# Performance work log

Measured on AMD Instinct MI355X. Metric: run time of the kernel, lower is better.

Reference implementation:

```python
import jax, jax.numpy as jnp
import numpy as np

C_CURV = 1.0
EPS = 1e-5            # bound_eps from source
MAX_NORM = (1.0 - 1e-5) / (C_CURV ** 0.5)  # Poincare ball projection radius


def _conv3x3(x, w, b):
    # x: (N,Cin,H,W), w: (Cout,Cin,3,3), padding=1 -> SAME
    y = jax.lax.conv_general_dilated(
        x, w, window_strides=(1, 1), padding=((1, 1), (1, 1)),
        dimension_numbers=('NCHW', 'OIHW', 'NCHW'))
    return y + b[None, :, None, None]


def _maxpool2(x):
    return jax.lax.reduce_window(x, -jnp.inf, jax.lax.max,
                                 (1, 1, 2, 2), (1, 1, 2, 2), 'VALID')


def _hyp_mlr(x, w, b):
    # x: (N,D), w: hyperplane_normals (K,D), b: hyperplane_offsets (K,D)
    c = C_CURV
    sqrt_c = c ** 0.5
    x2 = jnp.sum(x * x, axis=-1, keepdims=True)          # (N,1)
    b2 = jnp.sum(b * b, axis=-1)                          # (K,)
    w_norm = jnp.linalg.norm(w, axis=-1)                  # (K,)
    inner_x_b = x @ (-b.T)                                # (N,K)
    a_num = 1.0 + 2.0 * c * inner_x_b + c * x2            # (N,K)
    b_num = 1.0 - c * b2                                  # (K,)
    denom = 1.0 + 2.0 * c * inner_x_b + (c * c) * (x2 * b2[None, :])
    alpha = a_num / jnp.maximum(denom, EPS)
    beta = b_num[None, :] / denom                         # raw denom, as in source
    mob2 = alpha ** 2 * b2[None, :] + 2.0 * alpha * beta * inner_x_b + beta ** 2 * x2
    sq = jnp.sqrt(mob2)
    normalizer = jnp.where(sq > MAX_NORM, MAX_NORM / jnp.maximum(sq, EPS),
                           jnp.ones_like(mob2))
    mob2 = jnp.where(sq < MAX_NORM, mob2, jnp.full_like(mob2, MAX_NORM ** 2))
    wn = w / jnp.maximum(jnp.linalg.norm(w, axis=-1, keepdims=True), 1e-12)
    hyperplane = alpha * jnp.sum(wn * (-b), axis=-1)[None, :] + beta * (x @ wn.T)
    hyperplane = hyperplane * normalizer
    asinh_in = 2.0 * sqrt_c * hyperplane / jnp.maximum(1.0 - c * mob2, EPS)
    scaler = 2.0 / jnp.maximum(1.0 - c * b2, EPS)         # (K,)
    return (1.0 / sqrt_c) * (scaler * w_norm)[None, :] * jnp.arcsinh(asinh_in)


def setup_inputs() -> dict:
    key = jax.random.key(0)
    ks = jax.random.split(key, 8)
    N, D, K = 4096, 32, 10
    x = jax.random.normal(ks[0], (N, 1, 28, 28), dtype=jnp.float32)
    conv1_w = jax.random.normal(ks[1], (32, 1, 3, 3), dtype=jnp.float32) * 0.1
    conv1_b = jnp.zeros((32,), dtype=jnp.float32)
    conv2_w = jax.random.normal(ks[2], (64, 32, 3, 3), dtype=jnp.float32) * 0.05
    conv2_b = jnp.zeros((64,), dtype=jnp.float32)
    fc_w = jax.random.normal(ks[3], (D, 7 * 7 * 64), dtype=jnp.float32) * 0.02
    fc_b = jnp.zeros((D,), dtype=jnp.float32)
    hyp_w = jax.random.normal(ks[4], (K, D), dtype=jnp.float32) * 0.05
    hyp_b = jnp.zeros((K, D), dtype=jnp.float32)
    return dict(x=x, conv1_w=conv1_w, conv1_b=conv1_b, conv2_w=conv2_w,
                conv2_b=conv2_b, fc_w=fc_w, fc_b=fc_b, hyp_w=hyp_w, hyp_b=hyp_b)


def reference(x, conv1_w, conv1_b, conv2_w, conv2_b, fc_w, fc_b, hyp_w, hyp_b):
    h = _maxpool2(jax.nn.relu(_conv3x3(x, conv1_w, conv1_b)))   # (N,32,14,14)
    h = _maxpool2(jax.nn.relu(_conv3x3(h, conv2_w, conv2_b)))   # (N,64,7,7)
    h = h.reshape(h.shape[0], -1)                                # (N,3136)
    h = h @ fc_w.T + fc_b                                        # (N,32)
    return _hyp_mlr(h, hyp_w, hyp_b)                             # (N,10)
```

## Files before the change

kernel.cpp:

```cpp
#include <hip/hip_runtime.h>
#include <math.h>

#define EPSV 1e-5f

typedef _Float16 f16x8 __attribute__((ext_vector_type(8)));
typedef _Float16 f16x4 __attribute__((ext_vector_type(4)));
typedef float f32x4 __attribute__((ext_vector_type(4)));

__global__ __launch_bounds__(256) void prep_weights(
    const float* __restrict__ w1, const float* __restrict__ b1,
    const float* __restrict__ w2, const float* __restrict__ fw,
    _Float16* __restrict__ w2t_hi, _Float16* __restrict__ w2t_lo,
    _Float16* __restrict__ fw_hi,  _Float16* __restrict__ fw_lo,
    _Float16* __restrict__ w1p_hi, _Float16* __restrict__ w1p_lo)
{
    int idx = blockIdx.x * 256 + threadIdx.x;
    if (idx < 18432) {
        int off = idx >> 11;
        int rem = idx & 2047;
        int oc = rem >> 5, ic = rem & 31;
        float v = w2[(oc * 32 + ic) * 9 + off];
        _Float16 hx = (_Float16)v;
        w2t_hi[idx] = hx;
        w2t_lo[idx] = (_Float16)(v - (float)hx);
    } else if (idx < 18432 + 100352) {
        int j = idx - 18432;
        float v = fw[j];
        _Float16 hx = (_Float16)v;
        fw_hi[j] = hx;
        fw_lo[j] = (_Float16)(v - (float)hx);
    } else if (idx < 18432 + 100352 + 1024) {
        int j = idx - (18432 + 100352);
        int oc = j >> 5, k = j & 31;
        float v = (k < 9) ? w1[oc * 9 + k] : ((k == 9) ? b1[oc] : 0.f);
        _Float16 hx = (_Float16)v;
        w1p_hi[j] = hx;
        w1p_lo[j] = (_Float16)(v - (float)hx);
    }
}

template<int ROW0, int NROWS>
__device__ __forceinline__ void conv2_part(
    const _Float16* __restrict__ w2t_hi, const _Float16* __restrict__ w2t_lo,
    const _Float16* Bbuf_hi, const _Float16* Bbuf_lo,
    int oh, int cl, int clr, int kg,
    const float* __restrict__ b2, float pool[2][4][4])
{
    f32x4 acc[2][NROWS];
    #pragma unroll
    for (int j = 0; j < 2; ++j)
        #pragma unroll
        for (int pr = 0; pr < NROWS; ++pr) acc[j][pr] = (f32x4){0.f, 0.f, 0.f, 0.f};

    const size_t ar0 = (size_t)((2 * oh) * 16 + cl) * 32 + kg * 8;
    const size_t ar1 = (size_t)((2 * oh + 1) * 16 + cl) * 32 + kg * 8;
    f16x8 ah0 = *(const f16x8*)(w2t_hi + ar0);
    f16x8 al0 = *(const f16x8*)(w2t_lo + ar0);
    f16x8 ah1 = *(const f16x8*)(w2t_hi + ar1);
    f16x8 al1 = *(const f16x8*)(w2t_lo + ar1);

    #pragma unroll 1
    for (int off = 0; off < 9; ++off) {
        f16x8 nh0 = ah0, nl0 = al0, nh1 = ah1, nl1 = al1;
        if (off < 8) {
            const size_t d = (size_t)(off + 1) * 2048;
            nh0 = *(const f16x8*)(w2t_hi + ar0 + d);
            nl0 = *(const f16x8*)(w2t_lo + ar0 + d);
            nh1 = *(const f16x8*)(w2t_hi + ar1 + d);
            nl1 = *(const f16x8*)(w2t_lo + ar1 + d);
        }
        const int ky = off / 3, kx = off - ky * 3;
        const int cbase = (kg * 224 + clr + kx) * 8;
        __builtin_amdgcn_s_setprio(1);
        #pragma unroll
        for (int pr = 0; pr < NROWS; ++pr) {
            const int g = ROW0 + pr + ky;
            if (g >= 1 && g <= 14) {
                const int addr = cbase + (g - 1) * 128;
                f16x8 b_hi = *(const f16x8*)(Bbuf_hi + addr);
                f16x8 b_lo = *(const f16x8*)(Bbuf_lo + addr);
                acc[0][pr] = __builtin_amdgcn_mfma_f32_16x16x32_f16(ah0, b_hi, acc[0][pr], 0, 0, 0);
                acc[0][pr] = __builtin_amdgcn_mfma_f32_16x16x32_f16(al0, b_hi, acc[0][pr], 0, 0, 0);
                acc[0][pr] = __builtin_amdgcn_mfma_f32_16x16x32_f16(ah0, b_lo, acc[0][pr], 0, 0, 0);
                acc[1][pr] = __builtin_amdgcn_mfma_f32_16x16x32_f16(ah1, b_hi, acc[1][pr], 0, 0, 0);
                acc[1][pr] = __builtin_amdgcn_mfma_f32_16x16x32_f16(al1, b_hi, acc[1][pr], 0, 0, 0);
                acc[1][pr] = __builtin_amdgcn_mfma_f32_16x16x32_f16(ah1, b_lo, acc[1][pr], 0, 0, 0);
            }
        }
        __builtin_amdgcn_s_setprio(0);
        ah0 = nh0; al0 = nl0; ah1 = nh1; al1 = nl1;
    }
    #pragma unroll
    for (int j = 0; j < 2; ++j)
        #pragma unroll
        for (int pp = 0; pp < NROWS / 2; ++pp) {
            f32x4 r0 = acc[j][2 * pp], r1 = acc[j][2 * pp + 1];
            #pragma unroll
            for (int r = 0; r < 4; ++r) {
                const int oc = (2 * oh + j) * 16 + kg * 4 + r;
                float v0 = fmaxf(r0[r], __shfl_xor(r0[r], 1));
                float v1 = fmaxf(r1[r], __shfl_xor(r1[r], 1));
                pool[j][pp][r] = fmaxf(fmaxf(v0, v1) + b2[oc], 0.f);
            }
        }
}

__global__ __launch_bounds__(256, 4) void conv_fused(
    const float* __restrict__ x,
    const _Float16* __restrict__ w1p_hi,
    const _Float16* __restrict__ w1p_lo,
    const _Float16* __restrict__ w2t_hi,
    const _Float16* __restrict__ w2t_lo,
    const float* __restrict__ b2,
    _Float16* __restrict__ feat_hi,
    _Float16* __restrict__ feat_lo)
{
    __shared__ float4 smem4[2017];
    unsigned* in_pad  = (unsigned*)smem4;
    _Float16* Bbuf_hi = (_Float16*)((char*)smem4 + 3600);
    _Float16* Bbuf_lo = (_Float16*)((char*)smem4 + 17936);
    _Float16* Fhi     = (_Float16*)smem4;
    _Float16* Flo     = Fhi + 3136;

    const int tid  = threadIdx.x;
    const int lane = tid & 63;
    const int wave = tid >> 6;
    const int kg   = lane >> 4;
    const int cl   = lane & 15;
    const int clr  = (cl < 14) ? cl : 13;
    const int n    = blockIdx.x;

    for (int i = tid; i < 116; i += 256) {
        int yy, xx;
        if (i < 30)       { yy = 0;          xx = i; }
        else if (i < 60)  { yy = 29;         xx = i - 30; }
        else if (i < 88)  { yy = i - 60 + 1; xx = 0; }
        else              { yy = i - 88 + 1; xx = 29; }
        in_pad[yy * 30 + xx] = 0u;
    }
    const float* xin = x + (size_t)n * 784;
    for (int i = tid; i < 784; i += 256) {
        int yy = i / 28, xx = i - yy * 28;
        float v = xin[i];
        _Float16 hx = (_Float16)v;
        _Float16 lx = (_Float16)(v - (float)hx);
        unsigned hb = *(const unsigned short*)&hx;
        unsigned lb = *(const unsigned short*)&lx;
        in_pad[(yy + 1) * 30 + (xx + 1)] = hb | (lb << 16);
    }
    if (tid < 112) {
        int icg = tid / 28, j = tid - icg * 28;
        int row = j >> 1, col = (j & 1) ? 15 : 0;
        int c = (icg * 224 + row * 16 + col) * 8;
        *(f32x4*)(Bbuf_hi + c) = (f32x4){0.f, 0.f, 0.f, 0.f};
        *(f32x4*)(Bbuf_lo + c) = (f32x4){0.f, 0.f, 0.f, 0.f};
    }
    __syncthreads();

    {
        f16x8 a1h[2], a1l[2];
        #pragma unroll
        for (int m = 0; m < 2; ++m) {
            a1h[m] = *(const f16x8*)(w1p_hi + (m * 16 + cl) * 32 + kg * 8);
            a1l[m] = *(const f16x8*)(w1p_lo + (m * 16 + cl) * 32 + kg * 8);
        }
        const int o0 = (kg == 0) ? 0  : ((kg == 1) ? 62 : 0);
        const int o1 = (kg == 0) ? 1  : 0;
        const int o2 = (kg == 0) ? 2  : 0;
        const int o3 = (kg == 0) ? 30 : 0;
        const int o4 = (kg == 0) ? 31 : 0;
        const int o5 = (kg == 0) ? 32 : 0;
        const int o6 = (kg == 0) ? 60 : 0;
        const int o7 = (kg == 0) ? 61 : 0;

        const bool wr = ((cl & 1) == 0) && (cl < 14);

        #pragma unroll 1
        for (int u = 0; u < 7; ++u) {
            const int unit = wave * 7 + u;
            const int rp = unit >> 1, hx = unit & 1;
            const int xcol = hx * 14 + cl;
            f16x8 bh[2], bl[2];
            #pragma unroll
            for (int r2 = 0; r2 < 2; ++r2) {
                const int base = (2 * rp + r2) * 30 + xcol;
                unsigned v0 = in_pad[base + o0], v1 = in_pad[base + o1];
                unsigned v2 = in_pad[base + o2], v3 = in_pad[base + o3];
                unsigned v4 = in_pad[base + o4], v5 = in_pad[base + o5];
                unsigned v6 = in_pad[base + o6], v7 = in_pad[base + o7];
                unsigned h01 = (v0 & 0xFFFFu) | (v1 << 16);
                unsigned h23 = (v2 & 0xFFFFu) | (v3 << 16);
                unsigned h45 = (v4 & 0xFFFFu) | (v5 << 16);
                unsigned h67 = (v6 & 0xFFFFu) | (v7 << 16);
                unsigned l01 = (v0 >> 16) | (v1 & 0xFFFF0000u);
                unsigned l23 = (v2 >> 16) | (v3 & 0xFFFF0000u);
                unsigned l45 = (v4 >> 16) | (v5 & 0xFFFF0000u);
                unsigned l67 = (v6 >> 16) | (v7 & 0xFFFF0000u);
                if (kg == 1) {
                    h01 = (h01 & 0xFFFFu) | 0x3C000000u;
                    l01 = (l01 & 0xFFFFu);
                    h23 = h45 = h67 = 0u; l23 = l45 = l67 = 0u;
                } else if (kg >= 2) {
                    h01 = h23 = h45 = h67 = 0u;
                    l01 = l23 = l45 = l67 = 0u;
                }
                union { unsigned uu[4]; f16x8 v; } uh, ul;
                uh.uu[0] = h01; uh.uu[1] = h23; uh.uu[2] = h45; uh.uu[3] = h67;
                ul.uu[0] = l01; ul.uu[1] = l23; ul.uu[2] = l45; ul.uu[3] = l67;
                bh[r2] = uh.v; bl[r2] = ul.v;
            }
            #pragma unroll
            for (int m = 0; m < 2; ++m) {
                f32x4 a0 = (f32x4){0.f, 0.f, 0.f, 0.f};
                f32x4 a1 = (f32x4){0.f, 0.f, 0.f, 0.f};
                a0 = __builtin_amdgcn_mfma_f32_16x16x32_f16(a1h[m], bh[0], a0, 0, 0, 0);
                a0 = __builtin_amdgcn_mfma_f32_16x16x32_f16(a1l[m], bh[0], a0, 0, 0, 0);
                a0 = __builtin_amdgcn_mfma_f32_16x16x32_f16(a1h[m], bl[0], a0, 0, 0, 0);
                a1 = __builtin_amdgcn_mfma_f32_16x16x32_f16(a1h[m], bh[1], a1, 0, 0, 0);
                a1 = __builtin_amdgcn_mfma_f32_16x16x32_f16(a1l[m], bh[1], a1, 0, 0, 0);
                a1 = __builtin_amdgcn_mfma_f32_16x16x32_f16(a1h[m], bl[1], a1, 0, 0, 0);
                float pv[4];
                #pragma unroll
                for (int r = 0; r < 4; ++r) {
                    float vp = fmaxf(a0[r], a1[r]);
                    float hp = fmaxf(vp, __shfl_xor(vp, 1));
                    pv[r] = fmaxf(hp, 0.f);
                }
                union { unsigned short s[4]; f16x4 v; } ph, pl;
                #pragma unroll
                for (int r = 0; r < 4; ++r) {
                    _Float16 mh = (_Float16)pv[r];
                    _Float16 ml = (_Float16)(pv[r] - (float)mh);
                    ph.s[r] = *(const unsigned short*)&mh;
                    pl.s[r] = *(const unsigned short*)&ml;
                }
                if (wr) {
                    const int px2 = hx * 7 + (cl >> 1);
                    const int cell = ((m * 2 + (kg >> 1)) * 224 +
                                      rp * 16 + (px2 + 1)) * 8 + (kg & 1) * 4;
                    *(f16x4*)(Bbuf_hi + cell) = ph.v;
                    *(f16x4*)(Bbuf_lo + cell) = pl.v;
                }
            }
        }
    }
    __syncthreads();

    const int oh = wave & 1;
    const int rh = wave >> 1;

    float pool[2][4][4];
    if (rh == 0)
        conv2_part<0, 8>(w2t_hi, w2t_lo, Bbuf_hi, Bbuf_lo, oh, cl, clr, kg, b2, pool);
    else
        conv2_part<8, 6>(w2t_hi, w2t_lo, Bbuf_hi, Bbuf_lo, oh, cl, clr, kg, b2, pool);
    __syncthreads();

    {
        const bool wlane = ((cl & 1) == 0) && (cl < 14);
        const int px2 = cl >> 1;
        const int npp = (rh == 0) ? 4 : 3;
        #pragma unroll
        for (int j = 0; j < 2; ++j) {
            #pragma unroll
            for (int pp = 0; pp < 4; ++pp) {
                if (pp < npp) {
                    const int prow = rh * 4 + pp;
                    #pragma unroll
                    for (int r = 0; r < 4; ++r) {
                        const int oc = (2 * oh + j) * 16 + kg * 4 + r;
                        float mq = pool[j][pp][r];
                        _Float16 mh = (_Float16)mq;
                        _Float16 ml = (_Float16)(mq - (float)mh);
                        if (wlane) {
                            int o = oc * 49 + prow * 7 + px2;
                            Fhi[o] = mh; Flo[o] = ml;
                        }
                    }
                }
            }
        }
    }
    __syncthreads();

    unsigned* gh = (unsigned*)(feat_hi + (size_t)n * 3136);
    unsigned* gl = (unsigned*)(feat_lo + (size_t)n * 3136);
    const unsigned* sh = (const unsigned*)Fhi;
    const unsigned* sl = (const unsigned*)Flo;
    for (int i = tid; i < 1568; i += 256) { gh[i] = sh[i]; gl[i] = sl[i]; }
}

__global__ __launch_bounds__(512) void fc_mlr(
    const _Float16* __restrict__ feat_hi, const _Float16* __restrict__ feat_lo,
    const _Float16* __restrict__ fw_hi,   const _Float16* __restrict__ fw_lo,
    const float* __restrict__ fb,
    const float* __restrict__ hw,
    const float* __restrict__ hb,
    float* __restrict__ out)
{
    __shared__ float part[8][64][9];
    __shared__ float Ht[16][33];

    const int tid  = threadIdx.x;
    const int lane = tid & 63;
    const int wave = tid >> 6;
    const int kg = lane >> 4, cl = lane & 15;
    const int m0 = blockIdx.x * 16;

    const int start = (wave < 2) ? wave * 13 : 26 + (wave - 2) * 12;
    const int nstep = (wave < 2) ? 13 : 12;
    const size_t koff = (size_t)start * 32 + kg * 8;

    const _Float16* ah  = feat_hi + (size_t)(m0 + cl) * 3136 + koff;
    const _Float16* al  = feat_lo + (size_t)(m0 + cl) * 3136 + koff;
    const _Float16* b0h = fw_hi + (size_t)cl * 3136 + koff;
    const _Float16* b0l = fw_lo + (size_t)cl * 3136 + koff;
    const _Float16* b1h = fw_hi + (size_t)(16 + cl) * 3136 + koff;
    const _Float16* b1l = fw_lo + (size_t)(16 + cl) * 3136 + koff;

    f32x4 acc0 = {0.f, 0.f, 0.f, 0.f}, acc1 = {0.f, 0.f, 0.f, 0.f};
    for (int s = 0; s < nstep; ++s) {
        int k0 = s * 32;
        f16x8 vah = *(const f16x8*)(ah + k0);
        f16x8 val_ = *(const f16x8*)(al + k0);
        f16x8 v0h = *(const f16x8*)(b0h + k0);
        f16x8 v0l = *(const f16x8*)(b0l + k0);
        f16x8 v1h = *(const f16x8*)(b1h + k0);
        f16x8 v1l = *(const f16x8*)(b1l + k0);
        acc0 = __builtin_amdgcn_mfma_f32_16x16x32_f16(vah, v0h, acc0, 0, 0, 0);
        acc0 = __builtin_amdgcn_mfma_f32_16x16x32_f16(val_, v0h, acc0, 0, 0, 0);
        acc0 = __builtin_amdgcn_mfma_f32_16x16x32_f16(vah, v0l, acc0, 0, 0, 0);
        acc1 = __builtin_amdgcn_mfma_f32_16x16x32_f16(vah, v1h, acc1, 0, 0, 0);
        acc1 = __builtin_amdgcn_mfma_f32_16x16x32_f16(val_, v1h, acc1, 0, 0, 0);
        acc1 = __builtin_amdgcn_mfma_f32_16x16x32_f16(vah, v1l, acc1, 0, 0, 0);
    }
    #pragma unroll
    for (int r = 0; r < 4; ++r) {
        part[wave][lane][r]     = acc0[r];
        part[wave][lane][4 + r] = acc1[r];
    }
    __syncthreads();

    {
        int col = tid & 31, row = tid >> 5;
        int l  = ((row >> 2) << 4) + (col & 15);
        int rr = ((col >= 16) ? 4 : 0) + (row & 3);
        float s = 0.f;
        #pragma unroll
        for (int w = 0; w < 8; ++w) s += part[w][l][rr];
        Ht[row][col] = s + fb[col];
    }
    __syncthreads();

    if (tid < 160) {
        int im = tid / 10, k = tid - im * 10;
        const float* xr = &Ht[im][0];
        const float* wr = hw + k * 32;
        const float* br = hb + k * 32;
        float x2 = 0.f, b2s = 0.f, ww = 0.f, xb = 0.f, xw = 0.f, wb = 0.f;
        #pragma unroll
        for (int i = 0; i < 32; ++i) {
            float xi = xr[i], wi = wr[i], bi = br[i];
            x2 += xi * xi;  b2s += bi * bi;  ww += wi * wi;
            xb += xi * bi;  xw += xi * wi;   wb += wi * bi;
        }
        float w_norm = sqrtf(ww);
        float wnc = fmaxf(w_norm, 1e-12f);
        float inner = -xb;
        float a_num = 1.f + 2.f * inner + x2;
        float b_num = 1.f - b2s;
        float den = 1.f + 2.f * inner + x2 * b2s;
        float alpha = a_num / fmaxf(den, EPSV);
        float beta = b_num / den;
        float mob2 = alpha * alpha * b2s + 2.f * alpha * beta * inner + beta * beta * x2;
        float sq = sqrtf(mob2);
        const float MAXN = (float)(1.0 - 1e-5);
        const float MAXN2 = (float)((1.0 - 1e-5) * (1.0 - 1e-5));
        float normalizer = (sq > MAXN) ? (MAXN / fmaxf(sq, EPSV)) : 1.f;
        float mob2c = (sq < MAXN) ? mob2 : MAXN2;
        float hyper = (alpha * (-wb) + beta * xw) / wnc;
        hyper *= normalizer;
        float asin_in = 2.f * hyper / fmaxf(1.f - mob2c, EPSV);
        float scaler = 2.f / fmaxf(1.f - b2s, EPSV);
        out[(size_t)m0 * 10 + tid] = scaler * w_norm * asinhf(asin_in);
    }
}

extern "C" void kernel_launch(void* const* d_in, const int* in_sizes, int n_in,
                              void* d_out, int out_size, void* d_ws, size_t ws_size,
                              hipStream_t stream) {
    const float* x   = (const float*)d_in[0];
    const float* w1  = (const float*)d_in[1];
    const float* b1  = (const float*)d_in[2];
    const float* w2  = (const float*)d_in[3];
    const float* b2  = (const float*)d_in[4];
    const float* fw  = (const float*)d_in[5];
    const float* fb  = (const float*)d_in[6];
    const float* hw  = (const float*)d_in[7];
    const float* hb  = (const float*)d_in[8];
    float* out = (float*)d_out;

    const int N = 4096;
    char* ws = (char*)d_ws;
    _Float16* feat_hi = (_Float16*)ws;
    _Float16* feat_lo = (_Float16*)(ws + 25690112);
    _Float16* w2t_hi  = (_Float16*)(ws + 51380224);
    _Float16* w2t_lo  = (_Float16*)(ws + 51417088);
    _Float16* fw_hi   = (_Float16*)(ws + 51453952);
    _Float16* fw_lo   = (_Float16*)(ws + 51654656);
    _Float16* w1p_hi  = (_Float16*)(ws + 51855360);
    _Float16* w1p_lo  = (_Float16*)(ws + 51857408);

    prep_weights<<<(18432 + 100352 + 1024 + 255) / 256, 256, 0, stream>>>(
        w1, b1, w2, fw, w2t_hi, w2t_lo, fw_hi, fw_lo, w1p_hi, w1p_lo);
    conv_fused<<<N, 256, 0, stream>>>(x, w1p_hi, w1p_lo, w2t_hi, w2t_lo, b2,
                                      feat_hi, feat_lo);
    fc_mlr<<<N / 16, 512, 0, stream>>>(feat_hi, feat_lo, fw_hi, fw_lo, fb, hw, hb, out);
}
```

Measured before the change: 133.6 us.

## Fuse FC and hyperbolic MLR into conv kernel, drop feature round-trip

The FC layer and hyperbolic MLR now run at the end of the conv kernel, one image per block, instead of in a separate kernel. Features stay in shared memory, padded to 60 halves per channel, and each lane dot-products its channel against padded FC weights using fdot2 with hi/lo splitting, then reduces across the wave with shuffles. This removes the write and re-read of roughly 50 MB of hi/lo feature data and one kernel launch. In exchange, each block re-reads the whole FC weight matrix from cache, the reduction uses many shuffles, and the MLFMA-based FC is replaced by scalar dot2 work.

```diff
diff --git a/kernel.cpp b/kernel.cpp
--- a/kernel.cpp
+++ b/kernel.cpp
@@ -5,13 +5,14 @@
 
 typedef _Float16 f16x8 __attribute__((ext_vector_type(8)));
 typedef _Float16 f16x4 __attribute__((ext_vector_type(4)));
+typedef _Float16 f16x2 __attribute__((ext_vector_type(2)));
 typedef float f32x4 __attribute__((ext_vector_type(4)));
 
 __global__ __launch_bounds__(256) void prep_weights(
     const float* __restrict__ w1, const float* __restrict__ b1,
     const float* __restrict__ w2, const float* __restrict__ fw,
     _Float16* __restrict__ w2t_hi, _Float16* __restrict__ w2t_lo,
-    _Float16* __restrict__ fw_hi,  _Float16* __restrict__ fw_lo,
+    _Float16* __restrict__ fwp_hi, _Float16* __restrict__ fwp_lo,
     _Float16* __restrict__ w1p_hi, _Float16* __restrict__ w1p_lo)
 {
     int idx = blockIdx.x * 256 + threadIdx.x;
@@ -23,14 +24,17 @@
         _Float16 hx = (_Float16)v;
         w2t_hi[idx] = hx;
         w2t_lo[idx] = (_Float16)(v - (float)hx);
-    } else if (idx < 18432 + 100352) {
+    } else if (idx < 18432 + 114688) {
         int j = idx - 18432;
-        float v = fw[j];
+        int d = j / 3584;
+        int rem = j - d * 3584;
+        int oc = rem / 56, pos = rem - oc * 56;
+        float v = (pos < 49) ? fw[(size_t)d * 3136 + oc * 49 + pos] : 0.f;
         _Float16 hx = (_Float16)v;
-        fw_hi[j] = hx;
-        fw_lo[j] = (_Float16)(v - (float)hx);
-    } else if (idx < 18432 + 100352 + 1024) {
-        int j = idx - (18432 + 100352);
+        fwp_hi[j] = hx;
+        fwp_lo[j] = (_Float16)(v - (float)hx);
+    } else if (idx < 18432 + 114688 + 1024) {
+        int j = idx - (18432 + 114688);
         int oc = j >> 5, k = j & 31;
         float v = (k < 9) ? w1[oc * 9 + k] : ((k == 9) ? b1[oc] : 0.f);
         _Float16 hx = (_Float16)v;
@@ -112,15 +116,20 @@
     const _Float16* __restrict__ w2t_hi,
     const _Float16* __restrict__ w2t_lo,
     const float* __restrict__ b2,
-    _Float16* __restrict__ feat_hi,
-    _Float16* __restrict__ feat_lo)
+    const _Float16* __restrict__ fwp_hi,
+    const _Float16* __restrict__ fwp_lo,
+    const float* __restrict__ fb,
+    const float* __restrict__ hw,
+    const float* __restrict__ hb,
+    float* __restrict__ out)
 {
     __shared__ float4 smem4[2017];
     unsigned* in_pad  = (unsigned*)smem4;
     _Float16* Bbuf_hi = (_Float16*)((char*)smem4 + 3600);
     _Float16* Bbuf_lo = (_Float16*)((char*)smem4 + 17936);
     _Float16* Fhi     = (_Float16*)smem4;
-    _Float16* Flo     = Fhi + 3136;
+    _Float16* Flo     = Fhi + 3840;
+    float*    hbuf    = (float*)((char*)smem4 + 15360);
 
     const int tid  = threadIdx.x;
     const int lane = tid & 63;
@@ -144,9 +153,9 @@
         float v = xin[i];
         _Float16 hx = (_Float16)v;
         _Float16 lx = (_Float16)(v - (float)hx);
-        unsigned hb = *(const unsigned short*)&hx;
-        unsigned lb = *(const unsigned short*)&lx;
-        in_pad[(yy + 1) * 30 + (xx + 1)] = hb | (lb << 16);
+        unsigned hb_ = *(const unsigned short*)&hx;
+        unsigned lb_ = *(const unsigned short*)&lx;
+        in_pad[(yy + 1) * 30 + (xx + 1)] = hb_ | (lb_ << 16);
     }
     if (tid < 112) {
         int icg = tid / 28, j = tid - icg * 28;
@@ -273,88 +282,62 @@
                         _Float16 mh = (_Float16)mq;
                         _Float16 ml = (_Float16)(mq - (float)mh);
                         if (wlane) {
-                            int o = oc * 49 + prow * 7 + px2;
+                            int o = oc * 60 + prow * 7 + px2;
                             Fhi[o] = mh; Flo[o] = ml;
                         }
                     }
                 }
             }
         }
-    }
-    __syncthreads();
-
-    unsigned* gh = (unsigned*)(feat_hi + (size_t)n * 3136);
-    unsigned* gl = (unsigned*)(feat_lo + (size_t)n * 3136);
-    const unsigned* sh = (const unsigned*)Fhi;
-    const unsigned* sl = (const unsigned*)Flo;
-    for (int i = tid; i < 1568; i += 256) { gh[i] = sh[i]; gl[i] = sl[i]; }
-}
-
-__global__ __launch_bounds__(512) void fc_mlr(
-    const _Float16* __restrict__ feat_hi, const _Float16* __restrict__ feat_lo,
-    const _Float16* __restrict__ fw_hi,   const _Float16* __restrict__ fw_lo,
-    const float* __restrict__ fb,
-    const float* __restrict__ hw,
-    const float* __restrict__ hb,
-    float* __restrict__ out)
-{
-    __shared__ float part[8][64][9];
-    __shared__ float Ht[16][33];
-
-    const int tid  = threadIdx.x;
-    const int lane = tid & 63;
-    const int wave = tid >> 6;
-    const int kg = lane >> 4, cl = lane & 15;
-    const int m0 = blockIdx.x * 16;
-
-    const int start = (wave < 2) ? wave * 13 : 26 + (wave - 2) * 12;
-    const int nstep = (wave < 2) ? 13 : 12;
-    const size_t koff = (size_t)start * 32 + kg * 8;
-
-    const _Float16* ah  = feat_hi + (size_t)(m0 + cl) * 3136 + koff;
-    const _Float16* al  = feat_lo + (size_t)(m0 + cl) * 3136 + koff;
-    const _Float16* b0h = fw_hi + (size_t)cl * 3136 + koff;
-    const _Float16* b0l = fw_lo + (size_t)cl * 3136 + koff;
-    const _Float16* b1h = fw_hi + (size_t)(16 + cl) * 3136 + koff;
-    const _Float16* b1l = fw_lo + (size_t)(16 + cl) * 3136 + koff;
-
-    f32x4 acc0 = {0.f, 0.f, 0.f, 0.f}, acc1 = {0.f, 0.f, 0.f, 0.f};
-    for (int s = 0; s < nstep; ++s) {
-        int k0 = s * 32;
-        f16x8 vah = *(const f16x8*)(ah + k0);
-        f16x8 val_ = *(const f16x8*)(al + k0);
-        f16x8 v0h = *(const f16x8*)(b0h + k0);
-        f16x8 v0l = *(const f16x8*)(b0l + k0);
-        f16x8 v1h = *(const f16x8*)(b1h + k0);
-        f16x8 v1l = *(const f16x8*)(b1l + k0);
-        acc0 = __builtin_amdgcn_mfma_f32_16x16x32_f16(vah, v0h, acc0, 0, 0, 0);
-        acc0 = __builtin_amdgcn_mfma_f32_16x16x32_f16(val_, v0h, acc0, 0, 0, 0);
-        acc0 = __builtin_amdgcn_mfma_f32_16x16x32_f16(vah, v0l, acc0, 0, 0, 0);
-        acc1 = __builtin_amdgcn_mfma_f32_16x16x32_f16(vah, v1h, acc1, 0, 0, 0);
-        acc1 = __builtin_amdgcn_mfma_f32_16x16x32_f16(val_, v1h, acc1, 0, 0, 0);
-        acc1 = __builtin_amdgcn_mfma_f32_16x16x32_f16(vah, v1l, acc1, 0, 0, 0);
-    }
-    #pragma unroll
-    for (int r = 0; r < 4; ++r) {
-        part[wave][lane][r]     = acc0[r];
-        part[wave][lane][4 + r] = acc1[r];
+        for (int i = tid; i < 896; i += 256) {
+            int plane = i / 448, j = i - plane * 448;
+            int oc = j / 7, p = j - oc * 7;
+            (plane ? Flo : Fhi)[oc * 60 + 49 + p] = (_Float16)0.f;
+        }
     }
     __syncthreads();
 
     {
-        int col = tid & 31, row = tid >> 5;
-        int l  = ((row >> 2) << 4) + (col & 15);
-        int rr = ((col >= 16) ? 4 : 0) + (row & 3);
-        float s = 0.f;
-        #pragma unroll
-        for (int w = 0; w < 8; ++w) s += part[w][l][rr];
-        Ht[row][col] = s + fb[col];
-    }
-    __syncthreads();
-
-    if (tid < 160) {
-        int im = tid / 10, k = tid - im * 10;
-        const float* xr = &Ht[im][0];
+        f16x2 Fh[28], Fl[28];
+        {
+            const f16x2* fhp = (const f16x2*)(Fhi + lane * 60);
+            const f16x2* flp = (const f16x2*)(Flo + lane * 60);
+            #pragma unroll
+            for (int i = 0; i < 28; ++i) { Fh[i] = fhp[i]; Fl[i] = flp[i]; }
+        }
+        float hp[8];
+        #pragma unroll 1
+        for (int d = 0; d < 8; ++d) {
+            const int dd = wave * 8 + d;
+            const f16x2* whp = (const f16x2*)(fwp_hi + (size_t)dd * 3584 + lane * 56);
+            const f16x2* wlp = (const f16x2*)(fwp_lo + (size_t)dd * 3584 + lane * 56);
+            float s = 0.f;
+            #pragma unroll
+            for (int i = 0; i < 28; ++i) {
+                f16x2 a = whp[i], b = wlp[i];
+                s = __builtin_amdgcn_fdot2(Fh[i], a, s, false);
+                s = __builtin_amdgcn_fdot2(Fl[i], a, s, false);
+                s = __builtin_amdgcn_fdot2(Fh[i], b, s, false);
+            }
+            hp[d] = s;
+        }
+        #pragma unroll
+        for (int d = 0; d < 8; ++d) {
+            float v = hp[d];
+            #pragma unroll
+            for (int m = 1; m < 64; m <<= 1) v += __shfl_xor(v, m);
+            hp[d] = v;
+        }
+        if (lane == 0) {
+            #pragma unroll
+            for (int d = 0; d < 8; ++d) hbuf[wave * 8 + d] = hp[d] + fb[wave * 8 + d];
+        }
+    }
+    __syncthreads();
+
+    if (tid < 10) {
+        const int k = tid;
+        const float* xr = hbuf;
         const float* wr = hw + k * 32;
         const float* br = hb + k * 32;
         float x2 = 0.f, b2s = 0.f, ww = 0.f, xb = 0.f, xw = 0.f, wb = 0.f;
@@ -382,7 +365,7 @@
         hyper *= normalizer;
         float asin_in = 2.f * hyper / fmaxf(1.f - mob2c, EPSV);
         float scaler = 2.f / fmaxf(1.f - b2s, EPSV);
-        out[(size_t)m0 * 10 + tid] = scaler * w_norm * asinhf(asin_in);
+        out[(size_t)n * 10 + k] = scaler * w_norm * asinhf(asin_in);
     }
 }
 
@@ -402,18 +385,15 @@
 
     const int N = 4096;
     char* ws = (char*)d_ws;
-    _Float16* feat_hi = (_Float16*)ws;
-    _Float16* feat_lo = (_Float16*)(ws + 25690112);
-    _Float16* w2t_hi  = (_Float16*)(ws + 51380224);
-    _Float16* w2t_lo  = (_Float16*)(ws + 51417088);
-    _Float16* fw_hi   = (_Float16*)(ws + 51453952);
-    _Float16* fw_lo   = (_Float16*)(ws + 51654656);
-    _Float16* w1p_hi  = (_Float16*)(ws + 51855360);
-    _Float16* w1p_lo  = (_Float16*)(ws + 51857408);
-
-    prep_weights<<<(18432 + 100352 + 1024 + 255) / 256, 256, 0, stream>>>(
-        w1, b1, w2, fw, w2t_hi, w2t_lo, fw_hi, fw_lo, w1p_hi, w1p_lo);
+    _Float16* w2t_hi = (_Float16*)ws;
+    _Float16* w2t_lo = (_Float16*)(ws + 36864);
+    _Float16* fwp_hi = (_Float16*)(ws + 73728);
+    _Float16* fwp_lo = (_Float16*)(ws + 303104);
+    _Float16* w1p_hi = (_Float16*)(ws + 532480);
+    _Float16* w1p_lo = (_Float16*)(ws + 534528);
+
+    prep_weights<<<(18432 + 114688 + 1024 + 255) / 256, 256, 0, stream>>>(
+        w1, b1, w2, fw, w2t_hi, w2t_lo, fwp_hi, fwp_lo, w1p_hi, w1p_lo);
     conv_fused<<<N, 256, 0, stream>>>(x, w1p_hi, w1p_lo, w2t_hi, w2t_lo, b2,
-                                      feat_hi, feat_lo);
-    fc_mlr<<<N / 16, 512, 0, stream>>>(feat_hi, feat_lo, fw_hi, fw_lo, fb, hw, hb, out);
+                                      fwp_hi, fwp_lo, fb, hw, hb, out);
 }
```

Result: slower. 421.3 us (+215.5%).
